# Performance work log

Hardware: AMD Instinct MI355X
Metric: run time of the kernel (lower is better)

Reference implementation:

```python
import jax, jax.numpy as jnp
import numpy as np

B, L, D_MODEL = 8, 2048, 768
D_INNER, D_STATE, DT_RANK, K = 1536, 16, 48, 4


def setup_inputs() -> dict:
    key = jax.random.key(0)
    ks = jax.random.split(key, 9)
    s = 0.02
    return {
        "hidden_states": jax.random.normal(ks[0], (B, L, D_MODEL), jnp.float32),
        "W_in": jax.random.normal(ks[1], (D_MODEL, 2 * D_INNER), jnp.float32) * s,
        "conv_w": jax.random.normal(ks[2], (D_INNER, 1, K), jnp.float32) * s,
        "conv_b": jax.random.normal(ks[3], (D_INNER,), jnp.float32) * s,
        "W_x": jax.random.normal(ks[4], (DT_RANK + 2 * D_STATE, D_INNER), jnp.float32) * s,
        "W_dt": jax.random.normal(ks[5], (D_INNER, DT_RANK), jnp.float32) * s,
        "b_dt": jax.random.normal(ks[6], (D_INNER,), jnp.float32) * s,
        "A_log": jax.random.normal(ks[7], (D_INNER, D_STATE), jnp.float32),
        "D_param": jax.random.normal(ks[8], (D_INNER,), jnp.float32),
    }


def _mamba(hidden_states, W_in, conv_w, conv_b, W_x, W_dt, b_dt, A_log, D_param):
    # in_proj then chunk into ssm branch (x) and gating residual (res)
    xz = hidden_states @ W_in                      # (B, L, 2*d_inner)
    x, res = jnp.split(xz, 2, axis=-1)             # each (B, L, d_inner)

    # causal depthwise conv over time, then SiLU
    xc = x.transpose(0, 2, 1)                      # (B, C, L)
    xc = jax.lax.conv_general_dilated(
        xc, conv_w, window_strides=(1,), padding=[(K - 1, 0)],
        feature_group_count=D_INNER, dimension_numbers=("NCH", "OIH", "NCH"))
    x = jax.nn.silu(xc + conv_b[None, :, None]).transpose(0, 2, 1)  # (B, L, d_inner)

    # input-dependent SSM parameters
    x_dbl = x @ W_x.T                              # (B, L, dt_rank + 2*d_state)
    dt = jax.nn.softplus(x_dbl[..., :DT_RANK] @ W_dt.T + b_dt)      # (B, L, d_inner)
    Bm = x_dbl[..., DT_RANK:DT_RANK + D_STATE]     # (B, L, d_state)
    Cm = x_dbl[..., DT_RANK + D_STATE:]            # (B, L, d_state)
    A = -jnp.exp(A_log)                            # (d_inner, d_state)

    def step(h, inp):
        x_t, dt_t, B_t, C_t = inp                  # (B,d_inner),(B,d_inner),(B,d_state),(B,d_state)
        dA = jnp.exp(dt_t[..., None] * A)          # (B, d_inner, d_state)
        dBx = (dt_t * x_t)[..., None] * B_t[:, None, :]
        h = dA * h + dBx
        y = jnp.einsum("bds,bs->bd", h, C_t)
        return h, y

    xs = (x.transpose(1, 0, 2), dt.transpose(1, 0, 2),
          Bm.transpose(1, 0, 2), Cm.transpose(1, 0, 2))
    h0 = jnp.zeros((x.shape[0], D_INNER, D_STATE), x.dtype)
    _, ys = jax.lax.scan(step, h0, xs)             # ys: (L, B, d_inner)
    y = ys.transpose(1, 0, 2) + x * D_param        # skip term
    return y * jax.nn.silu(res)                    # gated output (B, L, d_inner)


def reference(hidden_states, W_in, conv_w, conv_b, W_x, W_dt, b_dt, A_log, D_param):
    return _mamba(hidden_states, W_in, conv_w, conv_b, W_x, W_dt, b_dt, A_log, D_param)
```

## Files before the change

kernel.cpp:

```cpp
#include <hip/hip_runtime.h>
#include <hip/hip_bf16.h>
#include <stdint.h>

#define B_SZ 8
#define L_SZ 2048
#define DM 768
#define DI 1536
#define DS 16
#define DR 48
#define M_SZ (B_SZ * L_SZ)
#define N1 (2 * DI)

#define NC 32
#define TC (L_SZ / NC)
#define CH (B_SZ * DI)
#define KS 6
#define NT2 (DM / 32)
#define L2E 1.44269504088896f

typedef short short8 __attribute__((ext_vector_type(8)));
typedef float f32x4 __attribute__((ext_vector_type(4)));
typedef float f32x2 __attribute__((ext_vector_type(2)));

__device__ __forceinline__ ushort f2b(float f) {
  __hip_bfloat16 h = __float2bfloat16(f);
  return *reinterpret_cast<ushort*>(&h);
}
__device__ __forceinline__ float b2f(ushort u) {
  __hip_bfloat16 h;
  *reinterpret_cast<ushort*>(&h) = u;
  return __bfloat162float(h);
}
__device__ __forceinline__ ushort f2h(float f) {
  _Float16 h = (_Float16)f;
  return *reinterpret_cast<ushort*>(&h);
}
__device__ __forceinline__ float h2f(ushort u) {
  _Float16 h;
  *reinterpret_cast<ushort*>(&h) = u;
  return (float)h;
}

__device__ __forceinline__ void gl16(const ushort* g, ushort* l) {
  __builtin_amdgcn_global_load_lds(
      (const __attribute__((address_space(1))) void*)g,
      (__attribute__((address_space(3))) void*)l, 16, 0, 0);
}


__global__ __launch_bounds__(256) void prep_all(const float4* __restrict__ hs4,
                                                const float* __restrict__ w_in,
                                                const float* __restrict__ wx_f,
                                                const float* __restrict__ wdt_f,
                                                ushort4* __restrict__ A1,
                                                ushort* __restrict__ wt,
                                                ushort* __restrict__ wx_b,
                                                ushort* __restrict__ wdt_p) {
  const int n4 = M_SZ * DM / 4;
  const int nT = 3072 * 96;
  const int nwx = 80 * DI;
  const int nwdt = DI * 64;
  int idx = blockIdx.x * 256 + threadIdx.x;
  if (idx < n4) {
    float4 v = hs4[idx];
    ushort4 o;
    o.x = f2b(v.x); o.y = f2b(v.y); o.z = f2b(v.z); o.w = f2b(v.w);
    A1[idx] = o;
  } else if (idx < n4 + nT) {
    int j = idx - n4;
    int n = j % 3072;
    int kb = (j / 3072) * 8;
    short8 o;
#pragma unroll
    for (int q = 0; q < 8; ++q) o[q] = (short)f2b(w_in[(size_t)(kb + q) * 3072 + n]);
    *(short8*)(wt + (size_t)n * DM + kb) = o;
  } else if (idx < n4 + nT + nwx) {
    int j = idx - n4 - nT;
    wx_b[j] = f2b(wx_f[j]);
  } else if (idx < n4 + nT + nwx + nwdt) {
    int j = idx - n4 - nT - nwx;
    int col = j >> 6, k = j & 63;
    wdt_p[j] = (k < DR) ? f2b(wdt_f[col * DR + k]) : (ushort)0;
  }
}


__global__ __launch_bounds__(512, 1) void gemm_xz(const ushort* __restrict__ A,
                                                  const ushort* __restrict__ Bt,
                                                  ushort* __restrict__ xout,
                                                  ushort* __restrict__ gateout) {
  __shared__ ushort lds[49152];

  const int t = threadIdx.x;
  const int lane = t & 63;
  const int wid = t >> 6;
  const int wm = wid >> 2, wn = wid & 3;
  const int r = lane & 15, hi = lane >> 4;

  const int g = blockIdx.x;
  const int xcd = g & 7;
  const int local = g >> 3;
  const int bx = xcd * 8 + local / 12;
  const int by = local % 12;
  const int bm = bx * 256;
  const int bn = by * 256;

  const ushort* gsrc[4];
  int ldso[4];
#pragma unroll
  for (int i = 0; i < 4; ++i) {
    int c = wid * 4 + i;
    if (c < 16)
      gsrc[i] = A + (size_t)(bm + c * 16 + r) * DM + hi * 8;
    else
      gsrc[i] = Bt + (size_t)(bn + (c - 16) * 16 + r) * DM + hi * 8;
    ldso[i] = c * 512;
  }

  f32x4 acc[8][4];
#pragma unroll
  for (int m = 0; m < 8; ++m)
#pragma unroll
    for (int n = 0; n < 4; ++n) acc[m][n] = f32x4{0.f, 0.f, 0.f, 0.f};

  ushort* b0 = lds;
  ushort* b1 = lds + 16384;
  ushort* b2 = lds + 32768;

#pragma unroll
  for (int i = 0; i < 4; ++i) gl16(gsrc[i], b0 + ldso[i]);
#pragma unroll
  for (int i = 0; i < 4; ++i) gl16(gsrc[i] + 32, b1 + ldso[i]);
  asm volatile("s_waitcnt vmcnt(4)" ::: "memory");
  __builtin_amdgcn_s_barrier();

  for (int kt = 0; kt < NT2; ++kt) {
    const bool stage = (kt + 2 < NT2);
    const int koff = (kt + 2) * 32;

    short8 bfr[4];
#pragma unroll
    for (int n = 0; n < 4; ++n)
      bfr[n] = *(const short8*)&b0[(16 + wn * 4 + n) * 512 + lane * 8];

#pragma unroll
    for (int q = 0; q < 2; ++q) {
      short8 afr[4];
#pragma unroll
      for (int m = 0; m < 4; ++m)
        afr[m] = *(const short8*)&b0[(wm * 8 + q * 4 + m) * 512 + lane * 8];

      if (stage) {
        gl16(gsrc[2 * q] + koff, b2 + ldso[2 * q]);
        gl16(gsrc[2 * q + 1] + koff, b2 + ldso[2 * q + 1]);
      }

      asm volatile("s_barrier" ::: "memory");

      __builtin_amdgcn_s_setprio(1);
#pragma unroll
      for (int m = 0; m < 4; ++m)
#pragma unroll
        for (int n = 0; n < 4; ++n)
          acc[q * 4 + m][n] =
              __builtin_amdgcn_mfma_f32_16x16x32_bf16(afr[m], bfr[n], acc[q * 4 + m][n], 0, 0, 0);
      __builtin_amdgcn_s_setprio(0);

      if (q == 1) {
        if (stage)
          asm volatile("s_waitcnt vmcnt(4)" ::: "memory");
        else
          asm volatile("s_waitcnt vmcnt(0)" ::: "memory");
      }
      asm volatile("s_barrier" ::: "memory");
    }

    ushort* tmp = b0; b0 = b1; b1 = b2; b2 = tmp;
  }

  const bool isx = (bn < DI);
  ushort* outp = isx ? xout : gateout;
  const int cbase = bn - (isx ? 0 : DI) + wn * 64;
#pragma unroll
  for (int mf = 0; mf < 8; ++mf)
#pragma unroll
    for (int nf = 0; nf < 4; ++nf) {
      int col = cbase + nf * 16 + r;
#pragma unroll
      for (int j = 0; j < 4; ++j) {
        int row = bm + wm * 128 + mf * 16 + hi * 4 + j;
        float v = acc[mf][nf][j];
        if (!isx) v = v / (1.f + __expf(-v));
        outp[(size_t)row * DI + col] = f2b(v);
      }
    }
}


__global__ __launch_bounds__(256) void conv_silu(const ushort* __restrict__ xp,
                                                 const float* __restrict__ cw,
                                                 const float* __restrict__ cb,
                                                 ushort* __restrict__ xc) {
  int tid = blockIdx.x * 256 + threadIdx.x;
  const int nd = DI / 8;
  int db = tid % nd;
  int row = tid / nd;
  int d0 = db * 8;
  int l = row & (L_SZ - 1);
  const ushort* base = xp + (size_t)row * DI + d0;
  short8 z8 = {0, 0, 0, 0, 0, 0, 0, 0};
  short8 x0 = *(const short8*)base;
  short8 xm1 = (l >= 1) ? *(const short8*)(base - DI) : z8;
  short8 xm2 = (l >= 2) ? *(const short8*)(base - 2 * DI) : z8;
  short8 xm3 = (l >= 3) ? *(const short8*)(base - 3 * DI) : z8;
  short8 o;
#pragma unroll
  for (int j = 0; j < 8; ++j) {
    float4 w = *(const float4*)(cw + (size_t)(d0 + j) * 4);
    float a = cb[d0 + j] + w.x * b2f((ushort)xm3[j]) + w.y * b2f((ushort)xm2[j]) +
              w.z * b2f((ushort)xm1[j]) + w.w * b2f((ushort)x0[j]);
    float s = a / (1.f + __expf(-a));
    o[j] = (short)f2b(s);
  }
  *(short8*)(xc + (size_t)row * DI + d0) = o;
}


__global__ __launch_bounds__(256) void xdbl_gemm(const ushort* __restrict__ xc,
                                                 const ushort* __restrict__ wx,
                                                 float* __restrict__ xdp) {
  int wave = blockIdx.x * 4 + (threadIdx.x >> 6);
  int ks = blockIdx.y;
  int lane = threadIdx.x & 63;
  int r = lane & 15, hi = lane >> 4;
  int row0 = wave * 16;
  f32x4 acc[5];
#pragma unroll
  for (int n = 0; n < 5; ++n) acc[n] = f32x4{0.f, 0.f, 0.f, 0.f};
  const int kbeg = ks * (DI / KS), kend = kbeg + DI / KS;
  for (int k0 = kbeg; k0 < kend; k0 += 32) {
    short8 a = *(const short8*)(xc + (size_t)(row0 + r) * DI + k0 + hi * 8);
#pragma unroll
    for (int n = 0; n < 5; ++n) {
      short8 b = *(const short8*)(wx + (size_t)(n * 16 + r) * DI + k0 + hi * 8);
      acc[n] = __builtin_amdgcn_mfma_f32_16x16x32_bf16(a, b, acc[n], 0, 0, 0);
    }
  }
  float* op = xdp + (size_t)ks * M_SZ * 80;
#pragma unroll
  for (int n = 0; n < 5; ++n)
#pragma unroll
    for (int j = 0; j < 4; ++j)
      op[(size_t)(row0 + hi * 4 + j) * 80 + n * 16 + r] = acc[n][j];
}

__global__ __launch_bounds__(256) void reduce_xd(const float4* __restrict__ xdp,
                                                 float4* __restrict__ xd) {
  int i = blockIdx.x * 256 + threadIdx.x;
  if (i >= M_SZ * 20) return;
  float4 s = xdp[i];
#pragma unroll
  for (int k = 1; k < KS; ++k) {
    float4 v = xdp[(size_t)k * M_SZ * 20 + i];
    s.x += v.x; s.y += v.y; s.z += v.z; s.w += v.w;
  }
  xd[i] = s;
}


__device__ __forceinline__ short8 pack8f(const float* p) {
  short8 v;
#pragma unroll
  for (int i = 0; i < 8; ++i) v[i] = (short)f2b(p[i]);
  return v;
}

__global__ __launch_bounds__(256) void dt_gemm(const float* __restrict__ xd,
                                               const ushort* __restrict__ wdtp,
                                               const float* __restrict__ bdt,
                                               ushort* __restrict__ dt) {
  int wave = blockIdx.x * 4 + (threadIdx.x >> 6);
  int lane = threadIdx.x & 63;
  int r = lane & 15, hi = lane >> 4;
  int row0 = wave * 16;
  int c0 = blockIdx.y * 64;

  float atmp[8];
  const float* ap = xd + (size_t)(row0 + r) * 80 + hi * 8;
  float4 q0 = *(const float4*)ap, q1 = *(const float4*)(ap + 4);
  atmp[0] = q0.x; atmp[1] = q0.y; atmp[2] = q0.z; atmp[3] = q0.w;
  atmp[4] = q1.x; atmp[5] = q1.y; atmp[6] = q1.z; atmp[7] = q1.w;
  short8 a0 = pack8f(atmp);
  short8 a1 = {0, 0, 0, 0, 0, 0, 0, 0};
  if (hi < 2) {
    const float* ap1 = xd + (size_t)(row0 + r) * 80 + 32 + hi * 8;
    float4 p0 = *(const float4*)ap1, p1 = *(const float4*)(ap1 + 4);
    atmp[0] = p0.x; atmp[1] = p0.y; atmp[2] = p0.z; atmp[3] = p0.w;
    atmp[4] = p1.x; atmp[5] = p1.y; atmp[6] = p1.z; atmp[7] = p1.w;
    a1 = pack8f(atmp);
  }

  f32x4 acc[4];
#pragma unroll
  for (int n = 0; n < 4; ++n) acc[n] = f32x4{0.f, 0.f, 0.f, 0.f};
#pragma unroll
  for (int n = 0; n < 4; ++n) {
    const ushort* wp = wdtp + (size_t)(c0 + n * 16 + r) * 64;
    short8 b0 = *(const short8*)(wp + hi * 8);
    short8 b1 = *(const short8*)(wp + 32 + hi * 8);
    acc[n] = __builtin_amdgcn_mfma_f32_16x16x32_bf16(a0, b0, acc[n], 0, 0, 0);
    acc[n] = __builtin_amdgcn_mfma_f32_16x16x32_bf16(a1, b1, acc[n], 0, 0, 0);
  }
#pragma unroll
  for (int n = 0; n < 4; ++n)
#pragma unroll
    for (int j = 0; j < 4; ++j) {
      int col = c0 + n * 16 + r;
      float z = acc[n][j] + bdt[col];
      float sp = (z > 20.f) ? z : __logf(1.f + __expf(z));
      dt[(size_t)(row0 + hi * 4 + j) * DI + col] = f2h(sp);
    }
}


__global__ __launch_bounds__(256) void scan_pass1(const ushort* __restrict__ dt,
                                                  const ushort* __restrict__ xc,
                                                  const float* __restrict__ xd,
                                                  const float* __restrict__ A_log,
                                                  float* __restrict__ hend,
                                                  float* __restrict__ sumdt) {
  const int d = blockIdx.x * 256 + threadIdx.x;
  const int c = blockIdx.y, b = blockIdx.z;
  const int t0 = c * TC;

  __shared__ float Bs[TC * 16];
  for (int i = threadIdx.x; i < TC * 16; i += 256) {
    int tt = i >> 4, s = i & 15;
    Bs[i] = xd[((size_t)(b * L_SZ + t0 + tt)) * 80 + DR + s];
  }

  f32x2 a2[8];
  const float4* al4 = (const float4*)(A_log + (size_t)d * DS);
#pragma unroll
  for (int q = 0; q < 4; ++q) {
    float4 v = al4[q];
    a2[2 * q] = f32x2{-__expf(v.x) * L2E, -__expf(v.y) * L2E};
    a2[2 * q + 1] = f32x2{-__expf(v.z) * L2E, -__expf(v.w) * L2E};
  }

  __syncthreads();

  f32x2 h2[8];
#pragma unroll
  for (int q = 0; q < 8; ++q) h2[q] = f32x2{0.f, 0.f};
  float sd = 0.f;

  const ushort* dtp = dt + ((size_t)b * L_SZ + t0) * DI + d;
  const ushort* xp = xc + ((size_t)b * L_SZ + t0) * DI + d;

  ushort dtu_n = *dtp;
  ushort xu_n = *xp;
  const f32x4* bp4 = (const f32x4*)Bs;
#pragma unroll 2
  for (int tt = 0; tt < TC; ++tt) {
    dtp += DI; xp += DI;
    ushort dtu = dtu_n;
    ushort xu = xu_n;
    dtu_n = *dtp;
    xu_n = *xp;
    float dtv = h2f(dtu);
    float xv = b2f(xu);
    sd += dtv;
    float dx = dtv * xv;
    f32x2 dts = f32x2{dtv, dtv};
    f32x2 dxs = f32x2{dx, dx};
#pragma unroll
    for (int q4 = 0; q4 < 4; ++q4) {
      f32x4 bq = bp4[q4];
#pragma unroll
      for (int hq = 0; hq < 2; ++hq) {
        int q = q4 * 2 + hq;
        f32x2 bv = f32x2{bq[2 * hq], bq[2 * hq + 1]};
        f32x2 arg, t2;
        asm("v_pk_mul_f32 %0, %1, %2" : "=v"(arg) : "v"(dts), "v"(a2[q]));
        float e0, e1;
        asm("v_exp_f32 %0, %1" : "=v"(e0) : "v"(arg[0]));
        asm("v_exp_f32 %0, %1" : "=v"(e1) : "v"(arg[1]));
        asm("v_pk_mul_f32 %0, %1, %2" : "=v"(t2) : "v"(dxs), "v"(bv));
        h2[q][0] = __builtin_fmaf(e0, h2[q][0], t2[0]);
        h2[q][1] = __builtin_fmaf(e1, h2[q][1], t2[1]);
      }
    }
    bp4 += 4;
  }

  const size_t ch = (size_t)b * DI + d;
  sumdt[ch * NC + c] = sd;
  f32x2* hp = (f32x2*)&hend[((size_t)c * CH + ch) * 16];
#pragma unroll
  for (int q = 0; q < 8; ++q) hp[q] = h2[q];
}

__global__ __launch_bounds__(256) void scan_pass2(const float* __restrict__ A_log,
                                                  const float* __restrict__ sumdt,
                                                  const float* __restrict__ hend,
                                                  float* __restrict__ hstart) {
  int idx = blockIdx.x * 256 + threadIdx.x;
  int ch = idx >> 4, s = idx & 15;
  int d = ch % DI;
  float A = -__expf(A_log[d * DS + s]);
  float h = 0.f;
  for (int c = 0; c < NC; ++c) {
    hstart[((size_t)c * CH + ch) * 16 + s] = h;
    float sd = sumdt[(size_t)ch * NC + c];
    h = __expf(A * sd) * h + hend[((size_t)c * CH + ch) * 16 + s];
  }
}

__global__ __launch_bounds__(256) void scan_pass3(const ushort* __restrict__ dt,
                                                  const ushort* __restrict__ xc,
                                                  const float* __restrict__ xd,
                                                  const ushort* __restrict__ gateb,
                                                  const float* __restrict__ A_log,
                                                  const float* __restrict__ Dp,
                                                  const float* __restrict__ hstart,
                                                  float* __restrict__ out) {
  const int d = blockIdx.x * 256 + threadIdx.x;
  const int c = blockIdx.y, b = blockIdx.z;
  const int t0 = c * TC;

  __shared__ float Bs[TC * 16];
  __shared__ float Cs[TC * 16];
  for (int i = threadIdx.x; i < TC * 16; i += 256) {
    int tt = i >> 4, s = i & 15;
    size_t row = ((size_t)(b * L_SZ + t0 + tt)) * 80;
    Bs[i] = xd[row + DR + s];
    Cs[i] = xd[row + DR + DS + s];
  }

  f32x2 a2[8];
  const float4* al4 = (const float4*)(A_log + (size_t)d * DS);
#pragma unroll
  for (int q = 0; q < 4; ++q) {
    float4 v = al4[q];
    a2[2 * q] = f32x2{-__expf(v.x) * L2E, -__expf(v.y) * L2E};
    a2[2 * q + 1] = f32x2{-__expf(v.z) * L2E, -__expf(v.w) * L2E};
  }
  const float Dpv = Dp[d];

  const size_t ch = (size_t)b * DI + d;
  f32x2 h2[8];
  const f32x2* hp = (const f32x2*)&hstart[((size_t)c * CH + ch) * 16];
#pragma unroll
  for (int q = 0; q < 8; ++q) h2[q] = hp[q];

  __syncthreads();

  const ushort* dtp = dt + ((size_t)b * L_SZ + t0) * DI + d;
  const ushort* xp = xc + ((size_t)b * L_SZ + t0) * DI + d;
  const ushort* gp = gateb + ((size_t)b * L_SZ + t0) * DI + d;
  float* op = out + ((size_t)b * L_SZ + t0) * DI + d;

  ushort dtu_n = *dtp;
  ushort xu_n = *xp;
  ushort gu_n = *gp;
  const f32x4* bp4 = (const f32x4*)Bs;
  const f32x4* cp4 = (const f32x4*)Cs;
#pragma unroll 2
  for (int tt = 0; tt < TC; ++tt) {
    dtp += DI; xp += DI; gp += DI;
    ushort dtu = dtu_n;
    ushort xu = xu_n;
    ushort gu = gu_n;
    dtu_n = *dtp;
    xu_n = *xp;
    gu_n = *gp;
    float dtv = h2f(dtu);
    float xv = b2f(xu);
    float gv = b2f(gu);
    float dx = dtv * xv;
    f32x2 dts = f32x2{dtv, dtv};
    f32x2 dxs = f32x2{dx, dx};
    f32x2 ya = f32x2{0.f, 0.f}, yb = f32x2{0.f, 0.f};
#pragma unroll
    for (int q4 = 0; q4 < 4; ++q4) {
      f32x4 bq = bp4[q4];
      f32x4 cq = cp4[q4];
#pragma unroll
      for (int hq = 0; hq < 2; ++hq) {
        int q = q4 * 2 + hq;
        f32x2 bv = f32x2{bq[2 * hq], bq[2 * hq + 1]};
        f32x2 cv = f32x2{cq[2 * hq], cq[2 * hq + 1]};
        f32x2 arg, t2;
        asm("v_pk_mul_f32 %0, %1, %2" : "=v"(arg) : "v"(dts), "v"(a2[q]));
        float e0, e1;
        asm("v_exp_f32 %0, %1" : "=v"(e0) : "v"(arg[0]));
        asm("v_exp_f32 %0, %1" : "=v"(e1) : "v"(arg[1]));
        asm("v_pk_mul_f32 %0, %1, %2" : "=v"(t2) : "v"(dxs), "v"(bv));
        h2[q][0] = __builtin_fmaf(e0, h2[q][0], t2[0]);
        h2[q][1] = __builtin_fmaf(e1, h2[q][1], t2[1]);
        if (hq)
          asm("v_pk_fma_f32 %0, %1, %2, %0" : "+v"(yb) : "v"(h2[q]), "v"(cv));
        else
          asm("v_pk_fma_f32 %0, %1, %2, %0" : "+v"(ya) : "v"(h2[q]), "v"(cv));
      }
    }
    bp4 += 4; cp4 += 4;
    float y = (ya[0] + ya[1]) + (yb[0] + yb[1]);
    op[0] = (y + xv * Dpv) * gv;
    op += DI;
  }
}


extern "C" void kernel_launch(void* const* d_in, const int* in_sizes, int n_in,
                              void* d_out, int out_size, void* d_ws, size_t ws_size,
                              hipStream_t stream) {
  const float* hs     = (const float*)d_in[0];
  const float* W_in   = (const float*)d_in[1];
  const float* conv_w = (const float*)d_in[2];
  const float* conv_b = (const float*)d_in[3];
  const float* W_x    = (const float*)d_in[4];
  const float* W_dt   = (const float*)d_in[5];
  const float* b_dt   = (const float*)d_in[6];
  const float* A_log  = (const float*)d_in[7];
  const float* D_par  = (const float*)d_in[8];
  float* out = (float*)d_out;
  char* ws = (char*)d_ws;

  size_t o = 0;
  ushort* A1   = (ushort*)(ws + o); o += (size_t)M_SZ * DM * 2;
  ushort* Wt1  = (ushort*)(ws + o); o += (size_t)N1 * DM * 2;
  ushort* xpre = (ushort*)(ws + o); o += (size_t)M_SZ * DI * 2;
  ushort* gate = (ushort*)(ws + o); o += (size_t)M_SZ * DI * 2;
  ushort* xcv  = (ushort*)(ws + o); o += (size_t)M_SZ * DI * 2;
  float*  xdbl = (float*)(ws + o);  o += (size_t)M_SZ * 80 * 4;
  ushort* dtb  = (ushort*)(ws + o); o += (size_t)M_SZ * DI * 2;
  float*  xdp  = (float*)(ws + o);  o += (size_t)KS * M_SZ * 80 * 4;
  ushort* Wxb  = (ushort*)(ws + o); o += (size_t)80 * DI * 2;
  ushort* Wdtp = (ushort*)(ws + o); o += (size_t)DI * 64 * 2;
  if (ws_size < o) return;

  float* hend   = (float*)(ws + 0);
  float* hstart = (float*)(ws + (size_t)NC * CH * 16 * 4);
  float* sumdt  = (float*)(ws + (size_t)2 * NC * CH * 16 * 4);

  const int nprep = M_SZ * DM / 4 + 3072 * 96 + 80 * DI + DI * 64;
  prep_all<<<dim3((nprep + 255) / 256), dim3(256), 0, stream>>>(
      (const float4*)hs, W_in, W_x, W_dt, (ushort4*)A1, Wt1, Wxb, Wdtp);

  gemm_xz<<<dim3((M_SZ / 256) * (N1 / 256)), dim3(512), 0, stream>>>(A1, Wt1, xpre, gate);

  conv_silu<<<dim3(M_SZ * DI / 8 / 256), dim3(256), 0, stream>>>(xpre, conv_w, conv_b, xcv);

  xdbl_gemm<<<dim3(M_SZ / 64, KS), dim3(256), 0, stream>>>(xcv, Wxb, xdp);
  reduce_xd<<<dim3((M_SZ * 20 + 255) / 256), dim3(256), 0, stream>>>((const float4*)xdp, (float4*)xdbl);

  dt_gemm<<<dim3(M_SZ / 64, 24), dim3(256), 0, stream>>>(xdbl, Wdtp, b_dt, dtb);

  scan_pass1<<<dim3(DI / 256, NC, B_SZ), dim3(256), 0, stream>>>(dtb, xcv, xdbl, A_log, hend, sumdt);
  scan_pass2<<<dim3(CH * 16 / 256), dim3(256), 0, stream>>>(A_log, sumdt, hend, hstart);
  scan_pass3<<<dim3(DI / 256, NC, B_SZ), dim3(256), 0, stream>>>(dtb, xcv, xdbl, gate,
                                                                 A_log, D_par, hstart, out);
}
```

Baseline: 415.9 us.

## Double scan chunk count, deepen load prefetch, and merge scan state buffers in place

Raises the number of time chunks in the chunked selective scan from 32 to 64, which doubles the number of scan blocks and shortens each block's serial recurrence. This is meant to improve occupancy and latency hiding in pass1 and pass3. Pass1 and pass3 now prefetch dt, x and gate two timesteps ahead instead of one, to hide global load latency. Pass2 rewrites the chunk-start states in place over a single buffer, so the workspace stays the same size with the doubled chunk count. The cost is a longer serial loop in pass2 and more state traffic between passes.

```diff
diff --git a/kernel.cpp b/kernel.cpp
--- a/kernel.cpp
+++ b/kernel.cpp
@@ -11,7 +11,7 @@
 #define M_SZ (B_SZ * L_SZ)
 #define N1 (2 * DI)
 
-#define NC 32
+#define NC 64
 #define TC (L_SZ / NC)
 #define CH (B_SZ * DI)
 #define KS 6
@@ -358,16 +358,16 @@
   const ushort* dtp = dt + ((size_t)b * L_SZ + t0) * DI + d;
   const ushort* xp = xc + ((size_t)b * L_SZ + t0) * DI + d;
 
-  ushort dtu_n = *dtp;
-  ushort xu_n = *xp;
+  ushort dt0 = dtp[0], dt1 = dtp[DI];
+  ushort xu0 = xp[0], xu1 = xp[DI];
+  dtp += 2 * (size_t)DI; xp += 2 * (size_t)DI;
   const f32x4* bp4 = (const f32x4*)Bs;
 #pragma unroll 2
   for (int tt = 0; tt < TC; ++tt) {
+    ushort dtu = dt0, xu = xu0;
+    dt0 = dt1; xu0 = xu1;
+    dt1 = *dtp; xu1 = *xp;
     dtp += DI; xp += DI;
-    ushort dtu = dtu_n;
-    ushort xu = xu_n;
-    dtu_n = *dtp;
-    xu_n = *xp;
     float dtv = h2f(dtu);
     float xv = b2f(xu);
     sd += dtv;
@@ -401,19 +401,21 @@
   for (int q = 0; q < 8; ++q) hp[q] = h2[q];
 }
 
+
 __global__ __launch_bounds__(256) void scan_pass2(const float* __restrict__ A_log,
                                                   const float* __restrict__ sumdt,
-                                                  const float* __restrict__ hend,
-                                                  float* __restrict__ hstart) {
+                                                  float* __restrict__ hbuf) {
   int idx = blockIdx.x * 256 + threadIdx.x;
   int ch = idx >> 4, s = idx & 15;
   int d = ch % DI;
   float A = -__expf(A_log[d * DS + s]);
   float h = 0.f;
   for (int c = 0; c < NC; ++c) {
-    hstart[((size_t)c * CH + ch) * 16 + s] = h;
+    float* p = &hbuf[((size_t)c * CH + ch) * 16 + s];
+    float he = *p;
+    *p = h;
     float sd = sumdt[(size_t)ch * NC + c];
-    h = __expf(A * sd) * h + hend[((size_t)c * CH + ch) * 16 + s];
+    h = __expf(A * sd) * h + he;
   }
 }
 
@@ -461,20 +463,18 @@
   const ushort* gp = gateb + ((size_t)b * L_SZ + t0) * DI + d;
   float* op = out + ((size_t)b * L_SZ + t0) * DI + d;
 
-  ushort dtu_n = *dtp;
-  ushort xu_n = *xp;
-  ushort gu_n = *gp;
+  ushort dt0 = dtp[0], dt1 = dtp[DI];
+  ushort xu0 = xp[0], xu1 = xp[DI];
+  ushort gu0 = gp[0], gu1 = gp[DI];
+  dtp += 2 * (size_t)DI; xp += 2 * (size_t)DI; gp += 2 * (size_t)DI;
   const f32x4* bp4 = (const f32x4*)Bs;
   const f32x4* cp4 = (const f32x4*)Cs;
 #pragma unroll 2
   for (int tt = 0; tt < TC; ++tt) {
+    ushort dtu = dt0, xu = xu0, gu = gu0;
+    dt0 = dt1; xu0 = xu1; gu0 = gu1;
+    dt1 = *dtp; xu1 = *xp; gu1 = *gp;
     dtp += DI; xp += DI; gp += DI;
-    ushort dtu = dtu_n;
-    ushort xu = xu_n;
-    ushort gu = gu_n;
-    dtu_n = *dtp;
-    xu_n = *xp;
-    gu_n = *gp;
     float dtv = h2f(dtu);
     float xv = b2f(xu);
     float gv = b2f(gu);
@@ -541,9 +541,8 @@
   ushort* Wdtp = (ushort*)(ws + o); o += (size_t)DI * 64 * 2;
   if (ws_size < o) return;
 
-  float* hend   = (float*)(ws + 0);
-  float* hstart = (float*)(ws + (size_t)NC * CH * 16 * 4);
-  float* sumdt  = (float*)(ws + (size_t)2 * NC * CH * 16 * 4);
+  float* hbuf  = (float*)(ws + 0);
+  float* sumdt = (float*)(ws + (size_t)NC * CH * 16 * 4);
 
   const int nprep = M_SZ * DM / 4 + 3072 * 96 + 80 * DI + DI * 64;
   prep_all<<<dim3((nprep + 255) / 256), dim3(256), 0, stream>>>(
@@ -558,8 +557,8 @@
 
   dt_gemm<<<dim3(M_SZ / 64, 24), dim3(256), 0, stream>>>(xdbl, Wdtp, b_dt, dtb);
 
-  scan_pass1<<<dim3(DI / 256, NC, B_SZ), dim3(256), 0, stream>>>(dtb, xcv, xdbl, A_log, hend, sumdt);
-  scan_pass2<<<dim3(CH * 16 / 256), dim3(256), 0, stream>>>(A_log, sumdt, hend, hstart);
+  scan_pass1<<<dim3(DI / 256, NC, B_SZ), dim3(256), 0, stream>>>(dtb, xcv, xdbl, A_log, hbuf, sumdt);
+  scan_pass2<<<dim3(CH * 16 / 256), dim3(256), 0, stream>>>(A_log, sumdt, hbuf);
   scan_pass3<<<dim3(DI / 256, NC, B_SZ), dim3(256), 0, stream>>>(dtb, xcv, xdbl, gate,
-                                                                 A_log, D_par, hstart, out);
-}
+                                                                 A_log, D_par, hbuf, out);
+}
```

Result: no change. 412.1 us (-0.9%).
